# Kernel optimization log

Measured on AMD Instinct MI355X. Metric: run time of the kernel, lower is better.

## Reference

```python
import jax, jax.numpy as jnp
import numpy as np

SEQ_LEN = 16384
ENC_H = 2048
DEC_H = 2048


def setup_inputs() -> dict:
    key = jax.random.key(0)
    k1, k2, k3 = jax.random.split(key, 3)
    encoder_hiddens = jax.random.normal(k1, (SEQ_LEN, ENC_H), dtype=jnp.float32)
    decoder_hidden = jax.random.normal(k2, (1, DEC_H), dtype=jnp.float32)
    W = jax.random.normal(k3, (ENC_H, DEC_H), dtype=jnp.float32) / np.sqrt(ENC_H)
    return {"encoder_hiddens": encoder_hiddens, "decoder_hidden": decoder_hidden, "W": W}


def reference(encoder_hiddens, decoder_hidden, W):
    # scores[s] = encoder_hiddens[s] @ W @ decoder_hidden^T  -> [S]
    scores = jnp.einsum('se,ed,od->s', encoder_hiddens, W, decoder_hidden)
    # exp + normalize == softmax over the sequence (stable form)
    weights = jax.nn.softmax(scores, axis=0)  # [S]
    # context = sum_s weights[s] * encoder_hiddens[s]  -> [1, ENC_H]
    context = jnp.einsum('s,se->e', weights, encoder_hiddens)[None, :]
    return context
```

## Files before the change

### kernel.cpp

```cpp
#include <hip/hip_runtime.h>

#define SEQ_LEN 16384
#define ENC_H   2048
#define DEC_H   2048
#define NB_SC   1024
#define NB_CTX  256
#define CHUNK   (SEQ_LEN / NB_CTX)
#define WTHR    1e-9f

__global__ __launch_bounds__(256) void k_wv(const float* __restrict__ W,
                                            const float* __restrict__ dec,
                                            float* __restrict__ v,
                                            float* __restrict__ out) {
    if (blockIdx.x < ENC_H / 256) out[blockIdx.x * 256 + threadIdx.x] = 0.f;
    const int wave = threadIdx.x >> 6, lane = threadIdx.x & 63;
    const int row  = blockIdx.x * 4 + wave;
    const float4* Wr = (const float4*)(W + (size_t)row * DEC_H);
    const float4* d4 = (const float4*)dec;
    float acc = 0.f;
#pragma unroll
    for (int k = 0; k < DEC_H / 4 / 64; ++k) {
        const int i = k * 64 + lane;
        const float4 w = Wr[i], d = d4[i];
        acc += w.x * d.x + w.y * d.y + w.z * d.z + w.w * d.w;
    }
#pragma unroll
    for (int off = 32; off > 0; off >>= 1) acc += __shfl_down(acc, off, 64);
    if (lane == 0) v[row] = acc;
}

__global__ __launch_bounds__(256) void k_scores(const float* __restrict__ enc,
                                                const float* __restrict__ v,
                                                float* __restrict__ scores,
                                                float* __restrict__ bmax,
                                                float* __restrict__ bsum) {
    __shared__ float4 sv[ENC_H / 4];
    __shared__ float smax[4], ssum[4];
    const float4* v4 = (const float4*)v;
    for (int i = threadIdx.x; i < ENC_H / 4; i += 256) sv[i] = v4[i];
    __syncthreads();

    const int wave = threadIdx.x >> 6, lane = threadIdx.x & 63;
    const int nw = gridDim.x * 4;
    float lm = -3.4e38f, lvals[4];
    int nv = 0;
    for (int row = blockIdx.x * 4 + wave; row < SEQ_LEN; row += nw) {
        const float4* er = (const float4*)(enc + (size_t)row * ENC_H);
        float acc = 0.f;
#pragma unroll
        for (int k = 0; k < ENC_H / 4 / 64; ++k) {
            const int i = k * 64 + lane;
            const float4 e = er[i], w = sv[i];
            acc += e.x * w.x + e.y * w.y + e.z * w.z + e.w * w.w;
        }
#pragma unroll
        for (int off = 32; off > 0; off >>= 1) acc += __shfl_down(acc, off, 64);
        if (lane == 0) { scores[row] = acc; lvals[nv++] = acc; lm = fmaxf(lm, acc); }
    }
    if (lane == 0) {
        float ls = 0.f;
        for (int k = 0; k < nv; ++k) ls += __expf(lvals[k] - lm);
        smax[wave] = lm; ssum[wave] = ls;
    }
    __syncthreads();
    if (threadIdx.x == 0) {
        float bm = fmaxf(fmaxf(smax[0], smax[1]), fmaxf(smax[2], smax[3]));
        float bs = 0.f;
        for (int w2 = 0; w2 < 4; ++w2) bs += ssum[w2] * __expf(smax[w2] - bm);
        bmax[blockIdx.x] = bm; bsum[blockIdx.x] = bs;
    }
}

__global__ __launch_bounds__(256) void k_ctx(const float* __restrict__ enc,
                                             const float* __restrict__ scores,
                                             const float* __restrict__ bmax,
                                             const float* __restrict__ bsum,
                                             float* __restrict__ out) {
    __shared__ float sred[4], sred2[4], sw[CHUNK];
    const int t = threadIdx.x, lane = t & 63, wave = t >> 6;

    float m = fmaxf(fmaxf(bmax[t], bmax[t + 256]), fmaxf(bmax[t + 512], bmax[t + 768]));
#pragma unroll
    for (int off = 32; off > 0; off >>= 1) m = fmaxf(m, __shfl_down(m, off, 64));
    if (lane == 0) sred[wave] = m;
    __syncthreads();
    m = fmaxf(fmaxf(sred[0], sred[1]), fmaxf(sred[2], sred[3]));

    float s = bsum[t]       * __expf(bmax[t]       - m)
            + bsum[t + 256] * __expf(bmax[t + 256] - m)
            + bsum[t + 512] * __expf(bmax[t + 512] - m)
            + bsum[t + 768] * __expf(bmax[t + 768] - m);
#pragma unroll
    for (int off = 32; off > 0; off >>= 1) s += __shfl_down(s, off, 64);
    if (lane == 0) sred2[wave] = s;
    __syncthreads();
    const float inv = 1.f / (sred2[0] + sred2[1] + sred2[2] + sred2[3]);

    const int b = blockIdx.x;
    if (t < CHUNK) sw[t] = __expf(scores[b * CHUNK + t] - m) * inv;
    __syncthreads();
    float wmax = 0.f;
    for (int r = 0; r < CHUNK; ++r) wmax = fmaxf(wmax, sw[r]);
    if (wmax <= WTHR) return;

    const float4* e4 = (const float4*)enc;
    float4 a0 = {0.f, 0.f, 0.f, 0.f}, a1 = {0.f, 0.f, 0.f, 0.f};
    const size_t base = (size_t)b * CHUNK * (ENC_H / 4);
    for (int r = 0; r < CHUNK; ++r) {
        const float w = sw[r];
        if (w <= WTHR) continue;
        const float4 e0 = e4[base + (size_t)r * (ENC_H / 4) + t];
        const float4 e1 = e4[base + (size_t)r * (ENC_H / 4) + t + 256];
        a0.x += w * e0.x; a0.y += w * e0.y; a0.z += w * e0.z; a0.w += w * e0.w;
        a1.x += w * e1.x; a1.y += w * e1.y; a1.z += w * e1.z; a1.w += w * e1.w;
    }
    atomicAdd(&out[4 * t + 0], a0.x);
    atomicAdd(&out[4 * t + 1], a0.y);
    atomicAdd(&out[4 * t + 2], a0.z);
    atomicAdd(&out[4 * t + 3], a0.w);
    atomicAdd(&out[4 * (t + 256) + 0], a1.x);
    atomicAdd(&out[4 * (t + 256) + 1], a1.y);
    atomicAdd(&out[4 * (t + 256) + 2], a1.z);
    atomicAdd(&out[4 * (t + 256) + 3], a1.w);
}

extern "C" void kernel_launch(void* const* d_in, const int* in_sizes, int n_in,
                              void* d_out, int out_size, void* d_ws, size_t ws_size,
                              hipStream_t stream) {
    const float* enc = (const float*)d_in[0];
    const float* dec = (const float*)d_in[1];
    const float* W   = (const float*)d_in[2];
    float* out = (float*)d_out;

    float* ws      = (float*)d_ws;
    float* v       = ws;
    float* scores  = v + ENC_H;
    float* bmax    = scores + SEQ_LEN;
    float* bsum    = bmax + NB_SC;

    k_wv    <<<ENC_H / 4, 256, 0, stream>>>(W, dec, v, out);
    k_scores<<<NB_SC,     256, 0, stream>>>(enc, v, scores, bmax, bsum);
    k_ctx   <<<NB_CTX,    256, 0, stream>>>(enc, scores, bmax, bsum, out);
}
```

Baseline: 209.8 us.

## Fuse three attention kernels into one persistent kernel with grid barriers

Merges the W·dec matvec, the score/partial-softmax pass and the weighted-context pass into a single launch of 1024 blocks. The stages are separated by a software grid barrier built on atomic counters, which are reset by a memset before the launch. The goal is to remove inter-kernel launch gaps and tail drains. The context stage now uses 1024 blocks of 16 rows each instead of 256 blocks of 64 rows, which adds parallelism but quadruples the output atomics. Correctness depends on all 1024 blocks being co-resident, and the spinning barrier adds its own overhead.

```diff
diff --git a/kernel.cpp b/kernel.cpp
--- a/kernel.cpp
+++ b/kernel.cpp
@@ -3,81 +3,87 @@
 #define SEQ_LEN 16384
 #define ENC_H   2048
 #define DEC_H   2048
-#define NB_SC   1024
-#define NB_CTX  256
-#define CHUNK   (SEQ_LEN / NB_CTX)
+#define NBLK    1024
+#define CHUNK   (SEQ_LEN / NBLK)
 #define WTHR    1e-9f
 
-__global__ __launch_bounds__(256) void k_wv(const float* __restrict__ W,
-                                            const float* __restrict__ dec,
-                                            float* __restrict__ v,
-                                            float* __restrict__ out) {
-    if (blockIdx.x < ENC_H / 256) out[blockIdx.x * 256 + threadIdx.x] = 0.f;
-    const int wave = threadIdx.x >> 6, lane = threadIdx.x & 63;
-    const int row  = blockIdx.x * 4 + wave;
-    const float4* Wr = (const float4*)(W + (size_t)row * DEC_H);
-    const float4* d4 = (const float4*)dec;
-    float acc = 0.f;
-#pragma unroll
-    for (int k = 0; k < DEC_H / 4 / 64; ++k) {
-        const int i = k * 64 + lane;
-        const float4 w = Wr[i], d = d4[i];
-        acc += w.x * d.x + w.y * d.y + w.z * d.z + w.w * d.w;
+__device__ __forceinline__ void gbar(int* cnt, int* gen) {
+    __syncthreads();
+    if (threadIdx.x == 0) {
+        const int g = __hip_atomic_load(gen, __ATOMIC_RELAXED, __HIP_MEMORY_SCOPE_AGENT);
+        const int prev = __hip_atomic_fetch_add(cnt, 1, __ATOMIC_ACQ_REL, __HIP_MEMORY_SCOPE_AGENT);
+        if (prev == NBLK - 1) {
+            __hip_atomic_fetch_add(gen, 1, __ATOMIC_RELEASE, __HIP_MEMORY_SCOPE_AGENT);
+        } else {
+            while (__hip_atomic_load(gen, __ATOMIC_ACQUIRE, __HIP_MEMORY_SCOPE_AGENT) == g)
+                __builtin_amdgcn_s_sleep(2);
+        }
     }
-#pragma unroll
-    for (int off = 32; off > 0; off >>= 1) acc += __shfl_down(acc, off, 64);
-    if (lane == 0) v[row] = acc;
+    __syncthreads();
 }
 
-__global__ __launch_bounds__(256) void k_scores(const float* __restrict__ enc,
-                                                const float* __restrict__ v,
-                                                float* __restrict__ scores,
-                                                float* __restrict__ bmax,
-                                                float* __restrict__ bsum) {
+__global__ __launch_bounds__(256, 4) void k_fused(
+    const float* __restrict__ enc, const float* __restrict__ dec,
+    const float* __restrict__ W, float* __restrict__ out,
+    float* v, float* scores, float* bmax, float* bsum, int* bar)
+{
     __shared__ float4 sv[ENC_H / 4];
-    __shared__ float smax[4], ssum[4];
-    const float4* v4 = (const float4*)v;
-    for (int i = threadIdx.x; i < ENC_H / 4; i += 256) sv[i] = v4[i];
-    __syncthreads();
+    __shared__ float sred[8];
+    __shared__ float sw[CHUNK];
+    const int t = threadIdx.x, lane = t & 63, wave = t >> 6;
+    const int b = blockIdx.x;
 
-    const int wave = threadIdx.x >> 6, lane = threadIdx.x & 63;
-    const int nw = gridDim.x * 4;
-    float lm = -3.4e38f, lvals[4];
-    int nv = 0;
-    for (int row = blockIdx.x * 4 + wave; row < SEQ_LEN; row += nw) {
-        const float4* er = (const float4*)(enc + (size_t)row * ENC_H);
+    if (b < ENC_H / 256) out[b * 256 + t] = 0.f;
+    if (wave < 2) {
+        const int row = b * 2 + wave;
+        const float4* Wr = (const float4*)(W + (size_t)row * DEC_H);
+        const float4* d4 = (const float4*)dec;
         float acc = 0.f;
 #pragma unroll
-        for (int k = 0; k < ENC_H / 4 / 64; ++k) {
+        for (int k = 0; k < DEC_H / 4 / 64; ++k) {
             const int i = k * 64 + lane;
-            const float4 e = er[i], w = sv[i];
-            acc += e.x * w.x + e.y * w.y + e.z * w.z + e.w * w.w;
+            const float4 w = Wr[i], d = d4[i];
+            acc += w.x * d.x + w.y * d.y + w.z * d.z + w.w * d.w;
         }
 #pragma unroll
         for (int off = 32; off > 0; off >>= 1) acc += __shfl_down(acc, off, 64);
-        if (lane == 0) { scores[row] = acc; lvals[nv++] = acc; lm = fmaxf(lm, acc); }
+        if (lane == 0) v[row] = acc;
     }
-    if (lane == 0) {
-        float ls = 0.f;
-        for (int k = 0; k < nv; ++k) ls += __expf(lvals[k] - lm);
-        smax[wave] = lm; ssum[wave] = ls;
+    gbar(&bar[0], &bar[2]);
+
+    {
+        const float4* v4 = (const float4*)v;
+        for (int i = t; i < ENC_H / 4; i += 256) sv[i] = v4[i];
+        __syncthreads();
+        float lm = -3.4e38f, lvals[4];
+        int nv = 0;
+        for (int row = b * 4 + wave; row < SEQ_LEN; row += NBLK * 4) {
+            const float4* er = (const float4*)(enc + (size_t)row * ENC_H);
+            float acc = 0.f;
+#pragma unroll
+            for (int k = 0; k < ENC_H / 4 / 64; ++k) {
+                const int i = k * 64 + lane;
+                const float4 e = er[i], w = sv[i];
+                acc += e.x * w.x + e.y * w.y + e.z * w.z + e.w * w.w;
+            }
+#pragma unroll
+            for (int off = 32; off > 0; off >>= 1) acc += __shfl_down(acc, off, 64);
+            if (lane == 0) { scores[row] = acc; lvals[nv++] = acc; lm = fmaxf(lm, acc); }
+        }
+        if (lane == 0) {
+            float ls = 0.f;
+            for (int k = 0; k < nv; ++k) ls += __expf(lvals[k] - lm);
+            sred[wave] = lm; sred[4 + wave] = ls;
+        }
+        __syncthreads();
+        if (t == 0) {
+            const float bm = fmaxf(fmaxf(sred[0], sred[1]), fmaxf(sred[2], sred[3]));
+            float bs = 0.f;
+            for (int w2 = 0; w2 < 4; ++w2) bs += sred[4 + w2] * __expf(sred[w2] - bm);
+            bmax[b] = bm; bsum[b] = bs;
+        }
     }
-    __syncthreads();
-    if (threadIdx.x == 0) {
-        float bm = fmaxf(fmaxf(smax[0], smax[1]), fmaxf(smax[2], smax[3]));
-        float bs = 0.f;
-        for (int w2 = 0; w2 < 4; ++w2) bs += ssum[w2] * __expf(smax[w2] - bm);
-        bmax[blockIdx.x] = bm; bsum[blockIdx.x] = bs;
-    }
-}
-
-__global__ __launch_bounds__(256) void k_ctx(const float* __restrict__ enc,
-                                             const float* __restrict__ scores,
-                                             const float* __restrict__ bmax,
-                                             const float* __restrict__ bsum,
-                                             float* __restrict__ out) {
-    __shared__ float sred[4], sred2[4], sw[CHUNK];
-    const int t = threadIdx.x, lane = t & 63, wave = t >> 6;
+    gbar(&bar[1], &bar[3]);
 
     float m = fmaxf(fmaxf(bmax[t], bmax[t + 256]), fmaxf(bmax[t + 512], bmax[t + 768]));
 #pragma unroll
@@ -85,21 +91,21 @@
     if (lane == 0) sred[wave] = m;
     __syncthreads();
     m = fmaxf(fmaxf(sred[0], sred[1]), fmaxf(sred[2], sred[3]));
-
+    __syncthreads();
     float s = bsum[t]       * __expf(bmax[t]       - m)
             + bsum[t + 256] * __expf(bmax[t + 256] - m)
             + bsum[t + 512] * __expf(bmax[t + 512] - m)
             + bsum[t + 768] * __expf(bmax[t + 768] - m);
 #pragma unroll
     for (int off = 32; off > 0; off >>= 1) s += __shfl_down(s, off, 64);
-    if (lane == 0) sred2[wave] = s;
+    if (lane == 0) sred[wave] = s;
     __syncthreads();
-    const float inv = 1.f / (sred2[0] + sred2[1] + sred2[2] + sred2[3]);
+    const float inv = 1.f / (sred[0] + sred[1] + sred[2] + sred[3]);
 
-    const int b = blockIdx.x;
     if (t < CHUNK) sw[t] = __expf(scores[b * CHUNK + t] - m) * inv;
     __syncthreads();
     float wmax = 0.f;
+#pragma unroll
     for (int r = 0; r < CHUNK; ++r) wmax = fmaxf(wmax, sw[r]);
     if (wmax <= WTHR) return;
 
@@ -132,13 +138,13 @@
     const float* W   = (const float*)d_in[2];
     float* out = (float*)d_out;
 
-    float* ws      = (float*)d_ws;
-    float* v       = ws;
-    float* scores  = v + ENC_H;
-    float* bmax    = scores + SEQ_LEN;
-    float* bsum    = bmax + NB_SC;
+    float* ws     = (float*)d_ws;
+    float* v      = ws;
+    float* scores = v + ENC_H;
+    float* bmax   = scores + SEQ_LEN;
+    float* bsum   = bmax + NBLK;
+    int*   bar    = (int*)(bsum + NBLK);
 
-    k_wv    <<<ENC_H / 4, 256, 0, stream>>>(W, dec, v, out);
-    k_scores<<<NB_SC,     256, 0, stream>>>(enc, v, scores, bmax, bsum);
-    k_ctx   <<<NB_CTX,    256, 0, stream>>>(enc, scores, bmax, bsum, out);
+    hipMemsetAsync(bar, 0, 4 * sizeof(int), stream);
+    k_fused<<<NBLK, 256, 0, stream>>>(enc, dec, W, out, v, scores, bmax, bsum, bar);
 }
```

Result: slower. 444.9 us (+112.0%).
